# Kernel optimization log

Measured on AMD Instinct MI355X. Metric: run time of the kernel, lower is better.

## Reference

```python
import jax, jax.numpy as jnp
import numpy as np

N = 100000
E = 50000
NNZ = 1000000
IN_CH = 128
H = 8
C = 16
NEG_SLOPE = 0.2


def setup_inputs() -> dict:
    key = jax.random.key(0)
    ks = jax.random.split(key, 9)
    stdv_w = np.sqrt(6.0 / (IN_CH + H * C))
    stdv_a = np.sqrt(6.0 / (H + C))
    return {
        "X": jax.random.normal(ks[0], (N, IN_CH), dtype=jnp.float32),
        "W_w": jax.random.uniform(ks[1], (IN_CH, H * C), minval=-stdv_w, maxval=stdv_w, dtype=jnp.float32),
        "W_b": jnp.zeros((H * C,), dtype=jnp.float32),
        "att_e": jax.random.uniform(ks[2], (4, H, C), minval=-stdv_a, maxval=stdv_a, dtype=jnp.float32),
        "att_v": jax.random.uniform(ks[3], (4, H, C), minval=-stdv_a, maxval=stdv_a, dtype=jnp.float32),
        "vertex": jax.random.randint(ks[4], (NNZ,), 0, N, dtype=jnp.int32),
        "edges": jax.random.randint(ks[5], (NNZ,), 0, E, dtype=jnp.int32),
        "e_class": jax.random.randint(ks[6], (NNZ,), 0, 4, dtype=jnp.int32),
        "v_class": jax.random.randint(ks[7], (NNZ,), 0, 4, dtype=jnp.int32),
    }


def _leaky_relu(x):
    return jnp.where(x >= 0, x, NEG_SLOPE * x)


def _segment_softmax(x, seg, num_segments):
    # numerically stable softmax over segments (torch_geometric style)
    m = jax.ops.segment_max(x, seg, num_segments=num_segments)
    ex = jnp.exp(x - m[seg])
    s = jax.ops.segment_sum(ex, seg, num_segments=num_segments)
    return ex / (s[seg] + 1e-16)


def reference(X, W_w, W_b, att_e, att_v, vertex, edges, e_class, v_class):
    # X: [N, IN_CH] -> [N, H, C]
    Xn = (X @ W_w + W_b).reshape(N, H, C)
    Xve = Xn[vertex]                                  # [NNZ, H, C] gather

    # vertex -> edge attention (edge-type-specific attention vectors)
    beta = _leaky_relu((Xve * att_e[e_class]).sum(-1))  # [NNZ, H]
    beta = _segment_softmax(beta, edges, E)
    Xe = jax.ops.segment_sum(Xve * beta[..., None], edges, num_segments=E)  # [E, H, C]

    # edge -> vertex attention (node-type-specific attention vectors)
    Xev = Xe[edges]                                   # [NNZ, H, C] gather
    alpha = _leaky_relu((Xev * att_v[v_class]).sum(-1))  # [NNZ, H]
    alpha = _segment_softmax(alpha, vertex, N)
    Xv = jax.ops.segment_sum(Xev * alpha[..., None], vertex, num_segments=N)  # [N, H, C]

    return jax.nn.relu(Xv.reshape(N, H * C))
```

## Files before the change

kernel.cpp:

```cpp
#include <hip/hip_runtime.h>
#include <math.h>

#define NN 100000
#define EE 50000
#define ZZ 1000000

#define NB    196
#define SPB_E 256
#define SPB_V 512
#define IPB   4096
#define CAP   8192

#define PART_BLOCKS  ((ZZ + IPB - 1) / IPB)
#define PART2_BLOCKS (2 * PART_BLOCKS)
#define GEMM_BLOCKS  ((NN + 63) / 64)
#define HIST_BLOCKS  512

typedef __attribute__((ext_vector_type(8))) short bf16x8;
typedef __attribute__((ext_vector_type(4))) float f32x4;

#if __has_builtin(__builtin_amdgcn_exp2f)
#define EXP2F(x) __builtin_amdgcn_exp2f(x)
#else
#define EXP2F(x) exp2f(x)
#endif
#if __has_builtin(__builtin_amdgcn_rcpf)
#define RCPF(x) __builtin_amdgcn_rcpf(x)
#else
#define RCPF(x) (1.f / (x))
#endif

__device__ __forceinline__ unsigned f2bf(float x) {
    const unsigned b = __float_as_uint(x);
    return (b + 0x7FFFu + ((b >> 16) & 1u)) >> 16;
}

__device__ __forceinline__ float xor1_add(float p) {
    return p + __int_as_float(__builtin_amdgcn_update_dpp(
        0, __float_as_int(p), 0xB1, 0xF, 0xF, true));
}

__global__ __launch_bounds__(256) void hist_wt(
    const int* __restrict__ vertex, const int* __restrict__ edges,
    unsigned* __restrict__ ghE, unsigned* __restrict__ ghV,
    const float* __restrict__ W, unsigned* __restrict__ Wtg)
{
    if (blockIdx.x >= HIST_BLOCKS) {
        const int b  = blockIdx.x - HIST_BLOCKS;
        const int n4 = threadIdx.x & 31;
        const int kp = b * 8 + (threadIdx.x >> 5);
        const float4* W4 = (const float4*)W;
        const float4 a = W4[(2 * kp) * 32 + n4];
        const float4 c = W4[(2 * kp + 1) * 32 + n4];
        Wtg[(4 * n4 + 0) * 68 + kp] = f2bf(a.x) | (f2bf(c.x) << 16);
        Wtg[(4 * n4 + 1) * 68 + kp] = f2bf(a.y) | (f2bf(c.y) << 16);
        Wtg[(4 * n4 + 2) * 68 + kp] = f2bf(a.z) | (f2bf(c.z) << 16);
        Wtg[(4 * n4 + 3) * 68 + kp] = f2bf(a.w) | (f2bf(c.w) << 16);
        return;
    }
    __shared__ unsigned hE[NB], hV[NB];
    for (int t = threadIdx.x; t < NB; t += 256) { hE[t] = 0; hV[t] = 0; }
    __syncthreads();
    const uint4* e4 = (const uint4*)edges;
    const uint4* v4 = (const uint4*)vertex;
    for (int i = blockIdx.x * 256 + threadIdx.x; i < ZZ / 4; i += HIST_BLOCKS * 256) {
        const uint4 e = e4[i];
        const uint4 v = v4[i];
        atomicAdd(&hE[e.x >> 8], 1u); atomicAdd(&hE[e.y >> 8], 1u);
        atomicAdd(&hE[e.z >> 8], 1u); atomicAdd(&hE[e.w >> 8], 1u);
        atomicAdd(&hV[v.x >> 9], 1u); atomicAdd(&hV[v.y >> 9], 1u);
        atomicAdd(&hV[v.z >> 9], 1u); atomicAdd(&hV[v.w >> 9], 1u);
    }
    __syncthreads();
    for (int t = threadIdx.x; t < NB; t += 256) {
        if (hE[t]) atomicAdd(&ghE[t], hE[t]);
        if (hV[t]) atomicAdd(&ghV[t], hV[t]);
    }
}

__device__ __forceinline__ void partition_side(
    unsigned* smem, int bid, bool isV,
    const int* __restrict__ vertex, const int* __restrict__ edges,
    const int* __restrict__ ecl, const int* __restrict__ vcl,
    const unsigned* __restrict__ ghE, const unsigned* __restrict__ ghV,
    unsigned* __restrict__ gcE, unsigned* __restrict__ gcV,
    unsigned* __restrict__ partE, unsigned* __restrict__ partV)
{
    unsigned* cur  = smem;
    unsigned* base = smem + 256;
    unsigned* sh   = smem + 512;
    const unsigned* gh = isV ? ghV : ghE;
    unsigned* gc   = isV ? gcV : gcE;
    unsigned* part = isV ? partV : partE;
    const int* key = isV ? vertex : edges;
    const int* pay = isV ? edges : vertex;
    const int* cls = isV ? vcl : ecl;
    const int  shb = isV ? 9 : 8;
    const unsigned mask = isV ? 511u : 255u;
    const int t = threadIdx.x;

    const unsigned g = (t < NB) ? gh[t] : 0u;
    sh[t] = g; __syncthreads();
    for (int o = 1; o < 256; o <<= 1) {
        const unsigned u = (t >= o) ? sh[t - o] : 0u; __syncthreads();
        sh[t] += u; __syncthreads();
    }
    base[t] = sh[t] - g;
    cur[t]  = 0u;
    __syncthreads();

    const int beg = bid * IPB;
    const int end = min(beg + IPB, ZZ);
    for (int i = beg + t; i < end; i += 256)
        atomicAdd(&cur[((unsigned)key[i]) >> shb], 1u);
    __syncthreads();
    for (int k = t; k < NB; k += 256) {
        const unsigned c = cur[k];
        cur[k] = c ? (base[k] + atomicAdd(&gc[k], c)) : 0u;
    }
    __syncthreads();
    for (int i = beg + t; i < end; i += 256) {
        const unsigned kk = (unsigned)key[i];
        const unsigned p = atomicAdd(&cur[kk >> shb], 1u);
        part[p] = (unsigned)pay[i] | (((unsigned)cls[i]) << 17) | ((kk & mask) << 19);
    }
}

__device__ __forceinline__ void gemm_body(
    unsigned* smem, int bid,
    const float* __restrict__ X, const unsigned* __restrict__ Wtg,
    const float* __restrict__ Bb, unsigned* __restrict__ outb)
{
    unsigned* Wt = smem;
    unsigned* Xl = smem + 4608;
    const int tid = threadIdx.x;
    const int wid = tid >> 6, lane = tid & 63;
    const int l16 = lane & 15, kg = lane >> 4;

    f32x4 acc[8];
#pragma unroll
    for (int nt = 0; nt < 8; ++nt) acc[nt] = (f32x4){0.f, 0.f, 0.f, 0.f};

#pragma unroll
    for (int h = 0; h < 2; ++h) {
        {
            const uint4* Wg4 = (const uint4*)Wtg;
            uint4* Wl4 = (uint4*)Wt;
#pragma unroll
            for (int i = 0; i < 4; ++i) {
                const int k = i * 256 + tid;
                const int n = k >> 3, c = k & 7;
                Wl4[n * 9 + c] = Wg4[n * 17 + h * 8 + c];
            }
        }
        {
            const float4* X4 = (const float4*)X;
            const size_t base = (size_t)bid * 2048;
#pragma unroll
            for (int i = 0; i < 4; ++i) {
                const int k = i * 256 + tid;
                const int row = k >> 4, q = k & 15;
                float4 v = make_float4(0.f, 0.f, 0.f, 0.f);
                if (bid * 64 + row < NN) v = X4[base + row * 32 + h * 16 + q];
                Xl[row * 36 + 2 * q]     = f2bf(v.x) | (f2bf(v.y) << 16);
                Xl[row * 36 + 2 * q + 1] = f2bf(v.z) | (f2bf(v.w) << 16);
            }
        }
        __syncthreads();
#pragma unroll
        for (int kt = 0; kt < 2; ++kt) {
            const bf16x8 a = *(const bf16x8*)&Xl[(16 * wid + l16) * 36 + kt * 16 + kg * 4];
#pragma unroll
            for (int nt = 0; nt < 8; ++nt) {
                const bf16x8 b = *(const bf16x8*)&Wt[(nt * 16 + l16) * 36 + kt * 16 + kg * 4];
                acc[nt] = __builtin_amdgcn_mfma_f32_16x16x32_bf16(a, b, acc[nt], 0, 0, 0);
            }
        }
        __syncthreads();
    }

    short* Xs = (short*)smem;
#pragma unroll
    for (int nt = 0; nt < 8; ++nt) {
        const float bc = Bb[nt * 16 + l16];
#pragma unroll
        for (int r = 0; r < 4; ++r) {
            const int rl = 16 * wid + kg * 4 + r;
            Xs[rl * 136 + nt * 16 + l16] = (short)f2bf(acc[nt][r] + bc);
        }
    }
    {
        const uint4* Xu = (const uint4*)smem;
        uint4* O = (uint4*)outb;
        const int rbase = bid * 64 + 16 * wid;
#pragma unroll
        for (int i = 0; i < 4; ++i) {
            const int f = i * 64 + lane;
            const int row = f >> 4, col = f & 15;
            const int grow = rbase + row;
            if (grow < NN)
                O[(size_t)grow * 16 + col] = Xu[(16 * wid + row) * 17 + col];
        }
    }
}

__global__ __launch_bounds__(256) void gemm_part(
    const float* __restrict__ X, const unsigned* __restrict__ Wtg,
    const float* __restrict__ Bb, unsigned* __restrict__ outb,
    const int* __restrict__ vertex, const int* __restrict__ edges,
    const int* __restrict__ ecl, const int* __restrict__ vcl,
    const unsigned* __restrict__ ghE, const unsigned* __restrict__ ghV,
    unsigned* __restrict__ gcE, unsigned* __restrict__ gcV,
    unsigned* __restrict__ partE, unsigned* __restrict__ partV)
{
    __shared__ unsigned smem[6912];
    if (blockIdx.x < PART2_BLOCKS) {
        const bool isV = blockIdx.x >= PART_BLOCKS;
        const int bid = isV ? (int)blockIdx.x - PART_BLOCKS : (int)blockIdx.x;
        partition_side(smem, bid, isV, vertex, edges, ecl, vcl,
                       ghE, ghV, gcE, gcV, partE, partV);
    } else {
        gemm_body(smem, blockIdx.x - PART2_BLOCKS, X, Wtg, Bb, outb);
    }
}

__global__ __launch_bounds__(256) void csr_build2(
    const unsigned* __restrict__ partE, const unsigned* __restrict__ partV,
    const unsigned* __restrict__ ghE, const unsigned* __restrict__ ghV,
    unsigned* __restrict__ offsE, unsigned* __restrict__ offsV,
    unsigned* __restrict__ csrE, unsigned* __restrict__ csrV)
{
    __shared__ unsigned hist[SPB_V];
    __shared__ unsigned thr[256];
    __shared__ unsigned loc[CAP];
    __shared__ unsigned begS, cntS;
    const bool isV = blockIdx.x >= NB;
    const unsigned* gh   = isV ? ghV : ghE;
    const unsigned* part = isV ? partV : partE;
    unsigned* offs = isV ? offsV : offsE;
    unsigned* csr  = isV ? csrV : csrE;
    const int spb  = isV ? SPB_V : SPB_E;
    const int nseg = isV ? NN : EE;
    const int b    = isV ? (int)blockIdx.x - NB : (int)blockIdx.x;
    const int t = threadIdx.x;

    unsigned g = (t < NB) ? gh[t] : 0u;
    thr[t] = g; __syncthreads();
    for (int o = 1; o < 256; o <<= 1) {
        const unsigned u = (t >= o) ? thr[t - o] : 0u; __syncthreads();
        thr[t] += u; __syncthreads();
    }
    if (t == b) { begS = thr[t] - g; cntS = min(g, (unsigned)CAP); }
    __syncthreads();
    const unsigned beg = begS, cnt = cntS;

    for (int k = t; k < spb; k += 256) hist[k] = 0;
    __syncthreads();
    for (unsigned i = t; i < cnt; i += 256)
        atomicAdd(&hist[(part[beg + i] >> 19) & (spb - 1)], 1u);
    __syncthreads();
    const int EL = spb >> 8;
    unsigned v[2] = {0u, 0u};
    unsigned tsum = 0;
    for (int k = 0; k < EL; ++k) { v[k] = hist[t * EL + k]; tsum += v[k]; }
    thr[t] = tsum; __syncthreads();
    for (int o = 1; o < 256; o <<= 1) {
        const unsigned u = (t >= o) ? thr[t - o] : 0u; __syncthreads();
        thr[t] += u; __syncthreads();
    }
    unsigned run = thr[t] - tsum;
    for (int k = 0; k < EL; ++k) {
        const int s = t * EL + k;
        const int gs = b * spb + s;
        if (gs <= nseg) offs[gs] = beg + run;
        hist[s] = run;
        run += v[k];
    }
    __syncthreads();
    for (unsigned i = t; i < cnt; i += 256) {
        const unsigned r = part[beg + i];
        const unsigned p = atomicAdd(&hist[(r >> 19) & (spb - 1)], 1u);
        if (p < (unsigned)CAP)
            loc[p] = (r & 0x1FFFFu) | (((r >> 17) & 3u) << 27);
    }
    __syncthreads();
    for (unsigned i = t; i < cnt; i += 256) csr[beg + i] = loc[i];
}

template <bool BF16OUT>
__global__ __launch_bounds__(256) void seg_att(
    const unsigned char* __restrict__ sb, const unsigned* __restrict__ offs,
    const unsigned* __restrict__ csr, const float* __restrict__ att,
    void* __restrict__ dst, int nseg)
{
    __shared__ float4 attl[132];
    if (threadIdx.x < 128) {
        const float4 a = ((const float4*)att)[threadIdx.x];
        const int cl = threadIdx.x >> 5, q = threadIdx.x & 31;
        attl[cl * 33 + q] = make_float4(a.x * 1.44269504f, a.y * 1.44269504f,
                                        a.z * 1.44269504f, a.w * 1.44269504f);
    }
    __syncthreads();
    const int lane = threadIdx.x & 63;
    const int qt   = lane >> 4;
    const int sl   = lane & 15;
    const int wseg = (blockIdx.x * 256 + threadIdx.x) >> 6;
    if (wseg >= nseg) return;
    const unsigned beg = offs[wseg], end = offs[wseg + 1];
    const unsigned sloff = (unsigned)(sl << 4);

    float s = 0.f;
    float a0 = 0.f, a1 = 0.f, a2 = 0.f, a3 = 0.f;
    float a4 = 0.f, a5 = 0.f, a6 = 0.f, a7 = 0.f;

    auto gat = [&](unsigned pk) -> uint4 {
        return *(const uint4*)(sb + (((pk & 0x07FFFFFFu) << 8) | sloff));
    };
    auto compute = [&](const uint4 u, unsigned pk, bool valid) {
        const float4 avA = attl[(pk >> 27) * 33 + 2 * sl];
        const float4 avB = attl[(pk >> 27) * 33 + 2 * sl + 1];
        const float x0 = __uint_as_float(u.x << 16);
        const float x1 = __uint_as_float(u.x & 0xFFFF0000u);
        const float x2 = __uint_as_float(u.y << 16);
        const float x3 = __uint_as_float(u.y & 0xFFFF0000u);
        const float x4 = __uint_as_float(u.z << 16);
        const float x5 = __uint_as_float(u.z & 0xFFFF0000u);
        const float x6 = __uint_as_float(u.w << 16);
        const float x7 = __uint_as_float(u.w & 0xFFFF0000u);
        float p = fmaf(x0, avA.x, fmaf(x1, avA.y, fmaf(x2, avA.z, fmaf(x3, avA.w,
                  fmaf(x4, avB.x, fmaf(x5, avB.y, fmaf(x6, avB.z, x7 * avB.w)))))));
        p = xor1_add(p);
        const float b = fmaxf(p, 0.2f * p);
        const float e = valid ? EXP2F(b) : 0.f;
        s += e;
        a0 = fmaf(x0, e, a0); a1 = fmaf(x1, e, a1);
        a2 = fmaf(x2, e, a2); a3 = fmaf(x3, e, a3);
        a4 = fmaf(x4, e, a4); a5 = fmaf(x5, e, a5);
        a6 = fmaf(x6, e, a6); a7 = fmaf(x7, e, a7);
    };

    unsigned jj = beg;
    const unsigned npair = (end - beg) >> 3;
    if (npair) {
        unsigned pk0 = csr[jj + qt];
        unsigned pk1 = csr[jj + 4 + qt];
        uint4 u0 = gat(pk0);
        uint4 u1 = gat(pk1);
        unsigned npk0 = csr[min(jj + 8 + (unsigned)qt, (unsigned)(ZZ - 1))];
        unsigned npk1 = csr[min(jj + 12 + (unsigned)qt, (unsigned)(ZZ - 1))];
        for (unsigned it = 0; it + 1 < npair; ++it) {
            const uint4 nu0 = gat(npk0);
            const uint4 nu1 = gat(npk1);
            const unsigned fj = jj + 16;
            const unsigned fpk0 = csr[min(fj + (unsigned)qt, (unsigned)(ZZ - 1))];
            const unsigned fpk1 = csr[min(fj + 4 + (unsigned)qt, (unsigned)(ZZ - 1))];
            compute(u0, pk0, true);
            compute(u1, pk1, true);
            pk0 = npk0; pk1 = npk1;
            u0 = nu0; u1 = nu1;
            npk0 = fpk0; npk1 = fpk1;
            jj += 8;
        }
        compute(u0, pk0, true);
        compute(u1, pk1, true);
        jj += 8;
    }
    for (; jj + 4 <= end; jj += 4) {
        const unsigned pk = csr[jj + qt];
        compute(gat(pk), pk, true);
    }
    if (jj < end) {
        const unsigned rem = end - jj;
        const unsigned j = min(jj + (unsigned)qt, end - 1);
        const unsigned pk = csr[j];
        compute(gat(pk), pk, (unsigned)qt < rem);
    }

    s  += __shfl_xor(s, 16);  s  += __shfl_xor(s, 32);
    a0 += __shfl_xor(a0, 16); a0 += __shfl_xor(a0, 32);
    a1 += __shfl_xor(a1, 16); a1 += __shfl_xor(a1, 32);
    a2 += __shfl_xor(a2, 16); a2 += __shfl_xor(a2, 32);
    a3 += __shfl_xor(a3, 16); a3 += __shfl_xor(a3, 32);
    a4 += __shfl_xor(a4, 16); a4 += __shfl_xor(a4, 32);
    a5 += __shfl_xor(a5, 16); a5 += __shfl_xor(a5, 32);
    a6 += __shfl_xor(a6, 16); a6 += __shfl_xor(a6, 32);
    a7 += __shfl_xor(a7, 16); a7 += __shfl_xor(a7, 32);

    const float inv = RCPF(s + 1e-16f);
    if (qt == 0) {
        const float o0 = a0 * inv, o1 = a1 * inv, o2 = a2 * inv, o3 = a3 * inv;
        const float o4 = a4 * inv, o5 = a5 * inv, o6 = a6 * inv, o7 = a7 * inv;
        if (BF16OUT) {
            uint4 r;
            r.x = f2bf(o0) | (f2bf(o1) << 16);
            r.y = f2bf(o2) | (f2bf(o3) << 16);
            r.z = f2bf(o4) | (f2bf(o5) << 16);
            r.w = f2bf(o6) | (f2bf(o7) << 16);
            ((uint4*)dst)[(size_t)wseg * 16 + sl] = r;
        } else {
            float4* O = (float4*)dst;
            O[(size_t)wseg * 32 + 2 * sl] =
                make_float4(fmaxf(o0, 0.f), fmaxf(o1, 0.f),
                            fmaxf(o2, 0.f), fmaxf(o3, 0.f));
            O[(size_t)wseg * 32 + 2 * sl + 1] =
                make_float4(fmaxf(o4, 0.f), fmaxf(o5, 0.f),
                            fmaxf(o6, 0.f), fmaxf(o7, 0.f));
        }
    }
}

extern "C" void kernel_launch(void* const* d_in, const int* in_sizes, int n_in,
                              void* d_out, int out_size, void* d_ws, size_t ws_size,
                              hipStream_t stream) {
    const float* X    = (const float*)d_in[0];
    const float* Ww   = (const float*)d_in[1];
    const float* Wb   = (const float*)d_in[2];
    const float* attE = (const float*)d_in[3];
    const float* attV = (const float*)d_in[4];
    const int* vertex = (const int*)d_in[5];
    const int* edges  = (const int*)d_in[6];
    const int* ecls   = (const int*)d_in[7];
    const int* vcls   = (const int*)d_in[8];
    float* out = (float*)d_out;

    char* w = (char*)d_ws;
    unsigned* ghE   = (unsigned*)(w);
    unsigned* ghV   = (unsigned*)(w + 1024);
    unsigned* gcE   = (unsigned*)(w + 2048);
    unsigned* gcV   = (unsigned*)(w + 3072);
    unsigned* offsE = (unsigned*)(w + 6144);
    unsigned* offsV = (unsigned*)(w + 206848);
    unsigned* csrE  = (unsigned*)(w + 606976);
    unsigned* csrV  = (unsigned*)(w + 4606976);
    unsigned* partE = (unsigned*)(w + 8606976);
    unsigned* partV = (unsigned*)(w + 12606976);
    unsigned* Wtg   = (unsigned*)(w + 21500000);
    unsigned* Xnb   = (unsigned*)d_out;
    unsigned* Xeb   = (unsigned*)(w + 8606976);

    hipMemsetAsync(d_ws, 0, 4096, stream);

    hist_wt<<<HIST_BLOCKS + 8, 256, 0, stream>>>(vertex, edges, ghE, ghV, Ww, Wtg);
    gemm_part<<<PART2_BLOCKS + GEMM_BLOCKS, 256, 0, stream>>>(
        X, Wtg, Wb, Xnb, vertex, edges, ecls, vcls, ghE, ghV, gcE, gcV, partE, partV);
    csr_build2<<<2 * NB, 256, 0, stream>>>(partE, partV, ghE, ghV,
                                           offsE, offsV, csrE, csrV);

    seg_att<true><<<(EE * 64 + 255) / 256, 256, 0, stream>>>(
        (const unsigned char*)Xnb, offsE, csrE, attE, Xeb, EE);

    seg_att<false><<<(NN * 64 + 255) / 256, 256, 0, stream>>>(
        (const unsigned char*)Xeb, offsV, csrV, attV, out, NN);
}
```

Before: 156.7 us.

## Stage partition output in LDS per bucket and vectorize key loads

The partition step now scatters packed entries into a shared-memory staging buffer grouped by bucket, using a local prefix scan, and then writes each bucket's run to global memory with contiguous per-wave copies. This replaces scattered single-word global writes. Key, payload and class arrays are also read as uint4 vectors. The cost is more LDS use, an extra scan with barriers, and an assumption that IPB and ZZ are multiples of 4.

```diff
diff --git a/kernel.cpp b/kernel.cpp
--- a/kernel.cpp
+++ b/kernel.cpp
@@ -86,9 +86,11 @@
     unsigned* __restrict__ gcE, unsigned* __restrict__ gcV,
     unsigned* __restrict__ partE, unsigned* __restrict__ partV)
 {
-    unsigned* cur  = smem;
-    unsigned* base = smem + 256;
-    unsigned* sh   = smem + 512;
+    unsigned* loc    = smem;
+    unsigned* cnt    = smem + 4096;
+    unsigned* lofs   = smem + 4352;
+    unsigned* gstart = smem + 4612;
+    unsigned* sh     = smem + 4868;
     const unsigned* gh = isV ? ghV : ghE;
     unsigned* gc   = isV ? gcV : gcE;
     unsigned* part = isV ? partV : partE;
@@ -105,24 +107,57 @@
         const unsigned u = (t >= o) ? sh[t - o] : 0u; __syncthreads();
         sh[t] += u; __syncthreads();
     }
-    base[t] = sh[t] - g;
-    cur[t]  = 0u;
+    const unsigned baset = sh[t] - g;
+    cnt[t] = 0u;
     __syncthreads();
 
     const int beg = bid * IPB;
     const int end = min(beg + IPB, ZZ);
-    for (int i = beg + t; i < end; i += 256)
-        atomicAdd(&cur[((unsigned)key[i]) >> shb], 1u);
-    __syncthreads();
-    for (int k = t; k < NB; k += 256) {
-        const unsigned c = cur[k];
-        cur[k] = c ? (base[k] + atomicAdd(&gc[k], c)) : 0u;
-    }
-    __syncthreads();
-    for (int i = beg + t; i < end; i += 256) {
-        const unsigned kk = (unsigned)key[i];
-        const unsigned p = atomicAdd(&cur[kk >> shb], 1u);
-        part[p] = (unsigned)pay[i] | (((unsigned)cls[i]) << 17) | ((kk & mask) << 19);
+    const uint4* key4 = (const uint4*)key;
+    for (int q = (beg >> 2) + t; q < (end >> 2); q += 256) {
+        const uint4 k4 = key4[q];
+        atomicAdd(&cnt[k4.x >> shb], 1u);
+        atomicAdd(&cnt[k4.y >> shb], 1u);
+        atomicAdd(&cnt[k4.z >> shb], 1u);
+        atomicAdd(&cnt[k4.w >> shb], 1u);
+    }
+    __syncthreads();
+    const unsigned c = cnt[t];
+    sh[t] = c; __syncthreads();
+    for (int o = 1; o < 256; o <<= 1) {
+        const unsigned u = (t >= o) ? sh[t - o] : 0u; __syncthreads();
+        sh[t] += u; __syncthreads();
+    }
+    lofs[t] = sh[t] - c;
+    if (t == 255) lofs[256] = sh[255];
+    gstart[t] = (t < NB && c) ? (baset + atomicAdd(&gc[t], c)) : 0u;
+    cnt[t] = 0u;
+    __syncthreads();
+    const uint4* pay4 = (const uint4*)pay;
+    const uint4* cls4 = (const uint4*)cls;
+    for (int q = (beg >> 2) + t; q < (end >> 2); q += 256) {
+        const uint4 k4 = key4[q];
+        const uint4 p4 = pay4[q];
+        const uint4 c4 = cls4[q];
+        unsigned b, r;
+        b = k4.x >> shb; r = atomicAdd(&cnt[b], 1u);
+        loc[lofs[b] + r] = p4.x | (c4.x << 17) | ((k4.x & mask) << 19);
+        b = k4.y >> shb; r = atomicAdd(&cnt[b], 1u);
+        loc[lofs[b] + r] = p4.y | (c4.y << 17) | ((k4.y & mask) << 19);
+        b = k4.z >> shb; r = atomicAdd(&cnt[b], 1u);
+        loc[lofs[b] + r] = p4.z | (c4.z << 17) | ((k4.z & mask) << 19);
+        b = k4.w >> shb; r = atomicAdd(&cnt[b], 1u);
+        loc[lofs[b] + r] = p4.w | (c4.w << 17) | ((k4.w & mask) << 19);
+    }
+    __syncthreads();
+    const int wid = t >> 6, lane = t & 63;
+    const int kend = min(wid * 49 + 49, NB);
+    for (int k = wid * 49; k < kend; ++k) {
+        const unsigned n  = lofs[k + 1] - lofs[k];
+        const unsigned g0 = gstart[k];
+        const unsigned l0 = lofs[k];
+        for (unsigned j = lane; j < n; j += 64)
+            part[g0 + j] = loc[l0 + j];
     }
 }
 
```

New measurement: 155.7 us. No clear change (-0.6%).
